# Performance work log

Measured on AMD Instinct MI355X. Metric: run time of the kernel, lower is better.

Reference implementation:

```python
import jax, jax.numpy as jnp
import numpy as np

H = 2880      # hidden_size
NH = 64       # num query heads
NKV = 8       # num kv heads
D = 64        # head_dim
G = NH // NKV # GQA group size
W = 128       # sliding window (keys per query, incl. self)
THETA = 150000.0
N = 1024      # tokens


def setup_inputs() -> dict:
    key = jax.random.key(0)
    k0, k1, k2, k3 = jax.random.split(key, 4)
    hidden_states = jax.random.normal(k0, (N, H), jnp.float32)
    Wqkv = jax.random.normal(k1, (H, (NH + 2 * NKV) * D), jnp.float32) * (H ** -0.5)
    Wo = jax.random.normal(k2, (NH * D, H), jnp.float32) * ((NH * D) ** -0.5)
    sinks = jax.random.normal(k3, (NH,), jnp.float32)
    positions = jnp.arange(N, dtype=jnp.int64)
    return {"hidden_states": hidden_states, "Wqkv": Wqkv, "Wo": Wo,
            "sinks": sinks, "positions": positions}


def _rope(x, pos):
    # NeoX-style rotary over full head_dim. x: [n, h, D], pos: [n]
    half = D // 2
    inv_freq = 1.0 / (THETA ** (jnp.arange(half, dtype=jnp.float32) / half))
    ang = pos[:, None].astype(jnp.float32) * inv_freq          # [n, half]
    cos = jnp.cos(ang)[:, None, :]
    sin = jnp.sin(ang)[:, None, :]
    x1, x2 = x[..., :half], x[..., half:]
    return jnp.concatenate([x1 * cos - x2 * sin, x2 * cos + x1 * sin], axis=-1)


def reference(hidden_states, Wqkv, Wo, sinks, positions):
    n = hidden_states.shape[0]
    qkv = hidden_states @ Wqkv
    q, k, v = jnp.split(qkv, [NH * D, NH * D + NKV * D], axis=-1)
    q = _rope(q.reshape(n, NH, D), positions)   # [n, NH, D]
    k = _rope(k.reshape(n, NKV, D), positions)  # [n, NKV, D]
    v = v.reshape(n, NKV, D)

    # Sliding-window key indices: query i attends keys j in [i-W+1, i]
    idx = positions[:, None] - (W - 1) + jnp.arange(W)[None, :]  # [n, W]
    valid = idx >= 0
    idx = jnp.clip(idx, 0, n - 1)
    k_win = k[idx]  # [n, W, NKV, D]
    v_win = v[idx]  # [n, W, NKV, D]

    qg = q.reshape(n, NKV, G, D)
    scores = jnp.einsum('nkgd,nwkd->nkgw', qg, k_win) * (D ** -0.5)
    scores = jnp.where(valid[:, None, None, :], scores, -jnp.inf)

    # Attention sinks: softmax over [scores, sink_logit]; sink gets no value.
    sink = sinks.reshape(NKV, G)                      # [NKV, G]
    m = jnp.maximum(scores.max(-1), sink[None])       # [n, NKV, G]
    p = jnp.exp(scores - m[..., None])                # [n, NKV, G, W]
    denom = p.sum(-1) + jnp.exp(sink[None] - m)       # [n, NKV, G]
    out = jnp.einsum('nkgw,nwkd->nkgd', p, v_win) / denom[..., None]
    return out.reshape(n, NH * D) @ Wo
```

## Files before the change

### kernel.cpp

```cpp
#include <hip/hip_runtime.h>
#include <hip/hip_bf16.h>

#define HDIM   2880
#define NH     64
#define NKV    8
#define DHEAD  64
#define GQ     (NH / NKV)
#define WIN    128
#define NTOK   1024
#define QKV_N  ((NH + 2 * NKV) * DHEAD)
#define QCOLS  (NH * DHEAD)
#define KOFF   QCOLS
#define VOFF   (QCOLS + NKV * DHEAD)
#define WO_PAD 2944

typedef __attribute__((ext_vector_type(8))) short short8;
typedef __attribute__((ext_vector_type(4))) float floatx4;

__device__ unsigned short g_Xb   [(size_t)NTOK  * HDIM];
__device__ float          g_qkv  [(size_t)NTOK  * QKV_N];
__device__ unsigned short g_attn [(size_t)NTOK  * QCOLS];
__device__ unsigned short g_WqkvT[(size_t)QKV_N * HDIM];
__device__ unsigned short g_WoT  [(size_t)WO_PAD * QCOLS];

__device__ __forceinline__ unsigned short f2b(float f) {
    __hip_bfloat16 h = __float2bfloat16(f);
    return *reinterpret_cast<unsigned short*>(&h);
}

__device__ __forceinline__ void gload_lds16(const unsigned short* g, unsigned short* l) {
    __builtin_amdgcn_global_load_lds(
        (const __attribute__((address_space(1))) unsigned int*)g,
        (__attribute__((address_space(3))) unsigned int*)l, 16, 0, 0);
}

__global__ __launch_bounds__(256) void transpose_cvt(
        const float* __restrict__ in, unsigned short* __restrict__ out,
        int K, int N) {
    int bk = blockIdx.x, bn = blockIdx.y;
    int t = threadIdx.x;
    __shared__ __align__(16) unsigned short T[64 * 72];
    #pragma unroll
    for (int i = 0; i < 4; ++i) {
        int c = i * 256 + t;
        int r = c >> 4, cc = (c & 15) * 4;
        float4 v = *(const float4*)(in + (size_t)(bk * 64 + r) * N + bn * 64 + cc);
        T[r * 72 + cc + 0] = f2b(v.x);
        T[r * 72 + cc + 1] = f2b(v.y);
        T[r * 72 + cc + 2] = f2b(v.z);
        T[r * 72 + cc + 3] = f2b(v.w);
    }
    __syncthreads();
    #pragma unroll
    for (int i = 0; i < 2; ++i) {
        int c = i * 256 + t;
        int rn = c >> 3, kc = (c & 7) * 8;
        int4 vv;
        unsigned short* tp = (unsigned short*)&vv;
        #pragma unroll
        for (int j = 0; j < 8; ++j) tp[j] = T[(kc + j) * 72 + rn];
        *(int4*)(out + (size_t)(bn * 64 + rn) * K + bk * 64 + kc) = vv;
    }
}

__global__ __launch_bounds__(256) void cvt_bf16(
        const float* __restrict__ in, unsigned short* __restrict__ out, int n4) {
    int id = blockIdx.x * 256 + threadIdx.x;
    if (id >= n4) return;
    float4 v = *(const float4*)(in + (size_t)id * 4);
    ushort4 o;
    o.x = f2b(v.x); o.y = f2b(v.y); o.z = f2b(v.z); o.w = f2b(v.w);
    *(ushort4*)(out + (size_t)id * 4) = o;
}

__global__ __launch_bounds__(256) void gemm64(
        const unsigned short* __restrict__ A, const unsigned short* __restrict__ Bt,
        float* __restrict__ C, int M, int N, int K) {
    int bm = blockIdx.x, bn = blockIdx.y;
    int t = threadIdx.x, lane = t & 63, wid = t >> 6;
    int quad = lane >> 4, ml = lane & 15;
    int wm = wid >> 1, wn = wid & 1;
    __shared__ __align__(16) unsigned short As[64 * 64];
    __shared__ __align__(16) unsigned short Bs[128 * 64];
    floatx4 acc[2][4];
    #pragma unroll
    for (int i = 0; i < 2; ++i)
        #pragma unroll
        for (int j = 0; j < 4; ++j) acc[i][j] = (floatx4){0.f, 0.f, 0.f, 0.f};

    int srow = lane >> 3;
    int scol = (lane & 7) * 8;
    const unsigned short* Ab = A  + (size_t)(bm * 64)  * K;
    const unsigned short* Bb = Bt + (size_t)(bn * 128) * K;

    for (int k0 = 0; k0 < K; k0 += 64) {
        #pragma unroll
        for (int j = 0; j < 2; ++j) {
            int grp = wid * 2 + j;
            int r = grp * 8 + srow;
            gload_lds16(Ab + (size_t)r * K + k0 + scol, &As[grp * 512]);
        }
        #pragma unroll
        for (int j = 0; j < 4; ++j) {
            int grp = wid * 4 + j;
            int r = grp * 8 + srow;
            gload_lds16(Bb + (size_t)r * K + k0 + scol, &Bs[grp * 512]);
        }
        __syncthreads();
        #pragma unroll
        for (int kk = 0; kk < 64; kk += 32) {
            short8 af[2], bf[4];
            #pragma unroll
            for (int mt = 0; mt < 2; ++mt)
                af[mt] = *(const short8*)&As[(wm * 32 + mt * 16 + ml) * 64 + kk + quad * 8];
            #pragma unroll
            for (int nt = 0; nt < 4; ++nt)
                bf[nt] = *(const short8*)&Bs[(wn * 64 + nt * 16 + ml) * 64 + kk + quad * 8];
            #pragma unroll
            for (int mt = 0; mt < 2; ++mt)
                #pragma unroll
                for (int nt = 0; nt < 4; ++nt)
                    acc[mt][nt] = __builtin_amdgcn_mfma_f32_16x16x32_bf16(af[mt], bf[nt], acc[mt][nt], 0, 0, 0);
        }
        __syncthreads();
    }
    #pragma unroll
    for (int mt = 0; mt < 2; ++mt)
        #pragma unroll
        for (int nt = 0; nt < 4; ++nt)
            #pragma unroll
            for (int r = 0; r < 4; ++r) {
                int row = bm * 64 + wm * 32 + mt * 16 + quad * 4 + r;
                int col = bn * 128 + wn * 64 + nt * 16 + ml;
                if (col < N) C[(size_t)row * N + col] = acc[mt][nt][r];
            }
}

__global__ __launch_bounds__(256) void rope_kernel(float* __restrict__ qkv) {
    int id = blockIdx.x * 256 + threadIdx.x;
    const int total = NTOK * (NH + NKV) * (DHEAD / 2);
    if (id >= total) return;
    int n = id / ((NH + NKV) * 32);
    int r = id - n * ((NH + NKV) * 32);
    int h = r >> 5, d = r & 31;
    int col = (h < NH) ? (h * DHEAD + d) : (KOFF + (h - NH) * DHEAD + d);
    size_t base = (size_t)n * QKV_N + col;
    float x1 = qkv[base];
    float x2 = qkv[base + 32];
    float inv = expf(-(float)d * 0.3724497053f);
    float ang = (float)n * inv;
    float s, c;
    sincosf(ang, &s, &c);
    qkv[base]      = x1 * c - x2 * s;
    qkv[base + 32] = x2 * c + x1 * s;
}

#define TQ     32
#define WROWS  160
#define KS_LD  72
#define VT_LD  168
#define PS_LD  168

__global__ __launch_bounds__(256) void attn_mfma(
        const float* __restrict__ qkv,
        const float* __restrict__ sinks,
        unsigned short* __restrict__ aout) {
    int t0 = blockIdx.x * TQ, kh = blockIdx.y;
    int t = threadIdx.x, lane = t & 63, wid = t >> 6;
    int quad = lane >> 4, ml = lane & 15;
    int wavebase = wid * 64;

    __shared__ __align__(16) unsigned short Ks[WROWS * KS_LD];
    __shared__ __align__(16) unsigned short Vt[DHEAD * VT_LD];
    __shared__ __align__(16) unsigned short Ps[4 * 16 * PS_LD];
    unsigned short* Psw = &Ps[wid * 16 * PS_LD];

    #pragma unroll
    for (int i = 0; i < 10; ++i) {
        int c = i * 256 + t;
        int w = c >> 4, dc = (c & 15) * 4;
        int r = t0 - 127 + w;
        r = min(max(r, 0), NTOK - 1);
        const float* kp = qkv + (size_t)r * QKV_N + KOFF + kh * DHEAD + dc;
        float4 kv = *(const float4*)kp;
        ushort4 kb;
        kb.x = f2b(kv.x); kb.y = f2b(kv.y); kb.z = f2b(kv.z); kb.w = f2b(kv.w);
        *(ushort4*)&Ks[w * KS_LD + dc] = kb;
        const float* vp = qkv + (size_t)r * QKV_N + VOFF + kh * DHEAD + dc;
        float4 vv = *(const float4*)vp;
        Vt[(dc + 0) * VT_LD + w] = f2b(vv.x);
        Vt[(dc + 1) * VT_LD + w] = f2b(vv.y);
        Vt[(dc + 2) * VT_LD + w] = f2b(vv.z);
        Vt[(dc + 3) * VT_LD + w] = f2b(vv.w);
    }
    __syncthreads();

    short8 qf[4][2];
    #pragma unroll
    for (int mt = 0; mt < 4; ++mt) {
        int m = wavebase + mt * 16 + ml;
        int tl = m & 31, g = m >> 5;
        const float* qp = qkv + (size_t)(t0 + tl) * QKV_N + (kh * GQ + g) * DHEAD;
        #pragma unroll
        for (int kk = 0; kk < 2; ++kk) {
            float4 a = *(const float4*)(qp + kk * 32 + quad * 8);
            float4 b = *(const float4*)(qp + kk * 32 + quad * 8 + 4);
            union { short8 s; unsigned short u[8]; } pk;
            pk.u[0] = f2b(a.x); pk.u[1] = f2b(a.y); pk.u[2] = f2b(a.z); pk.u[3] = f2b(a.w);
            pk.u[4] = f2b(b.x); pk.u[5] = f2b(b.y); pk.u[6] = f2b(b.z); pk.u[7] = f2b(b.w);
            qf[mt][kk] = pk.s;
        }
    }

    floatx4 S[4][10];
    #pragma unroll
    for (int mt = 0; mt < 4; ++mt)
        #pragma unroll
        for (int nt = 0; nt < 10; ++nt) S[mt][nt] = (floatx4){0.f, 0.f, 0.f, 0.f};
    #pragma unroll
    for (int kk = 0; kk < 2; ++kk) {
        #pragma unroll
        for (int nt = 0; nt < 10; ++nt) {
            short8 kb = *(const short8*)&Ks[(nt * 16 + ml) * KS_LD + kk * 32 + quad * 8];
            #pragma unroll
            for (int mt = 0; mt < 4; ++mt)
                S[mt][nt] = __builtin_amdgcn_mfma_f32_16x16x32_bf16(qf[mt][kk], kb, S[mt][nt], 0, 0, 0);
        }
    }

    int wmin0 = 127 - t0;
    #pragma unroll
    for (int mt = 0; mt < 4; ++mt) {
        #pragma unroll
        for (int r = 0; r < 4; ++r) {
            int tl = (wavebase + mt * 16 + quad * 4 + r) & 31;
            int wlo = tl > wmin0 ? tl : wmin0;
            int whi = tl + 127;
            #pragma unroll
            for (int nt = 0; nt < 10; ++nt) {
                int w = nt * 16 + ml;
                float s = S[mt][nt][r] * 0.125f;
                S[mt][nt][r] = (w >= wlo && w <= whi) ? s : -INFINITY;
            }
        }
    }

    #pragma unroll
    for (int mt = 0; mt < 4; ++mt) {
        int g = (wavebase + mt * 16) >> 5;
        float sk = sinks[kh * GQ + g];
        #pragma unroll
        for (int r = 0; r < 4; ++r) {
            float rm = -INFINITY;
            #pragma unroll
            for (int nt = 0; nt < 10; ++nt) rm = fmaxf(rm, S[mt][nt][r]);
            #pragma unroll
            for (int off = 1; off < 16; off <<= 1) rm = fmaxf(rm, __shfl_xor(rm, off));
            rm = fmaxf(rm, sk);
            float sum = 0.f;
            #pragma unroll
            for (int nt = 0; nt < 10; ++nt) {
                float p = __expf(S[mt][nt][r] - rm);
                S[mt][nt][r] = p;
                sum += p;
            }
            #pragma unroll
            for (int off = 1; off < 16; off <<= 1) sum += __shfl_xor(sum, off);
            float inv = 1.f / (sum + __expf(sk - rm));
            #pragma unroll
            for (int nt = 0; nt < 10; ++nt) S[mt][nt][r] *= inv;
        }
    }

    #pragma unroll
    for (int mt = 0; mt < 4; ++mt) {
        int m = wavebase + mt * 16;
        #pragma unroll
        for (int r = 0; r < 4; ++r) {
            int lr = quad * 4 + r;
            #pragma unroll
            for (int nt = 0; nt < 10; ++nt)
                Psw[lr * PS_LD + nt * 16 + ml] = f2b(S[mt][nt][r]);
        }
        floatx4 O[4];
        #pragma unroll
        for (int j = 0; j < 4; ++j) O[j] = (floatx4){0.f, 0.f, 0.f, 0.f};
        #pragma unroll
        for (int ks = 0; ks < 5; ++ks) {
            short8 pf = *(const short8*)&Psw[ml * PS_LD + ks * 32 + quad * 8];
            #pragma unroll
            for (int nt = 0; nt < 4; ++nt) {
                short8 vf = *(const short8*)&Vt[(nt * 16 + ml) * VT_LD + ks * 32 + quad * 8];
                O[nt] = __builtin_amdgcn_mfma_f32_16x16x32_bf16(pf, vf, O[nt], 0, 0, 0);
            }
        }
        #pragma unroll
        for (int r = 0; r < 4; ++r) {
            int mm = m + quad * 4 + r;
            int tl = mm & 31, g = mm >> 5;
            unsigned short* op = aout + (size_t)(t0 + tl) * QCOLS + (kh * GQ + g) * DHEAD;
            #pragma unroll
            for (int nt = 0; nt < 4; ++nt)
                op[nt * 16 + ml] = f2b(O[nt][r]);
        }
    }
}

extern "C" void kernel_launch(void* const* d_in, const int* in_sizes, int n_in,
                              void* d_out, int out_size, void* d_ws, size_t ws_size,
                              hipStream_t stream) {
    const float* X     = (const float*)d_in[0];
    const float* Wqkv  = (const float*)d_in[1];
    const float* Wo    = (const float*)d_in[2];
    const float* sinks = (const float*)d_in[3];
    float* out = (float*)d_out;

    unsigned short *Xb = nullptr, *attn = nullptr, *WqkvT = nullptr, *WoT = nullptr;
    float *qkv = nullptr;
    hipGetSymbolAddress((void**)&Xb,    HIP_SYMBOL(g_Xb));
    hipGetSymbolAddress((void**)&qkv,   HIP_SYMBOL(g_qkv));
    hipGetSymbolAddress((void**)&attn,  HIP_SYMBOL(g_attn));
    hipGetSymbolAddress((void**)&WqkvT, HIP_SYMBOL(g_WqkvT));
    hipGetSymbolAddress((void**)&WoT,   HIP_SYMBOL(g_WoT));

    cvt_bf16<<<(NTOK * HDIM / 4 + 255) / 256, 256, 0, stream>>>(X, Xb, NTOK * HDIM / 4);
    transpose_cvt<<<dim3(HDIM / 64, QKV_N / 64), 256, 0, stream>>>(Wqkv, WqkvT, HDIM, QKV_N);
    transpose_cvt<<<dim3(QCOLS / 64, HDIM / 64), 256, 0, stream>>>(Wo, WoT, QCOLS, HDIM);

    gemm64<<<dim3(NTOK / 64, QKV_N / 128), 256, 0, stream>>>(Xb, WqkvT, qkv, NTOK, QKV_N, HDIM);

    rope_kernel<<<(NTOK * (NH + NKV) * 32) / 256, 256, 0, stream>>>(qkv);

    attn_mfma<<<dim3(NTOK / TQ, NKV), 256, 0, stream>>>(qkv, sinks, attn);

    gemm64<<<dim3(NTOK / 64, WO_PAD / 128), 256, 0, stream>>>(attn, WoT, out, NTOK, HDIM, QCOLS);
}
```

Measured before the change: 348.5 us.

## Split-K GEMMs with fused reduce+RoPE, bf16 qkv, smaller attention tiles

Both GEMMs now use 128x128 tiles with split-K (3 and 4 slices) writing fp32 partial planes. A separate reduce kernel sums the partials, and for the QKV projection it also applies RoPE and stores qkv as bf16. Attention reads the bf16 qkv directly and uses 16-token tiles, giving twice as many blocks. The aim is more parallelism on a small-M problem and less fp32 qkv traffic, at the cost of extra partial-buffer writes and reads plus reduction launches.

New measurement: 333.0 us. 1.05x faster.

```diff
diff --git a/kernel.cpp b/kernel.cpp
--- a/kernel.cpp
+++ b/kernel.cpp
@@ -13,15 +13,19 @@
 #define KOFF   QCOLS
 #define VOFF   (QCOLS + NKV * DHEAD)
 #define WO_PAD 2944
+#define SK1    3
+#define SK2    4
 
 typedef __attribute__((ext_vector_type(8))) short short8;
 typedef __attribute__((ext_vector_type(4))) float floatx4;
 
 __device__ unsigned short g_Xb   [(size_t)NTOK  * HDIM];
-__device__ float          g_qkv  [(size_t)NTOK  * QKV_N];
+__device__ unsigned short g_qkvb [(size_t)NTOK  * QKV_N];
 __device__ unsigned short g_attn [(size_t)NTOK  * QCOLS];
 __device__ unsigned short g_WqkvT[(size_t)QKV_N * HDIM];
 __device__ unsigned short g_WoT  [(size_t)WO_PAD * QCOLS];
+__device__ float          g_part1[(size_t)SK1 * NTOK * QKV_N];
+__device__ float          g_part2[(size_t)SK2 * NTOK * WO_PAD];
 
 __device__ __forceinline__ unsigned short f2b(float f) {
     __hip_bfloat16 h = __float2bfloat16(f);
@@ -73,102 +77,151 @@
     *(ushort4*)(out + (size_t)id * 4) = o;
 }
 
-__global__ __launch_bounds__(256) void gemm64(
+__global__ __launch_bounds__(256) void gemm_sk(
         const unsigned short* __restrict__ A, const unsigned short* __restrict__ Bt,
-        float* __restrict__ C, int M, int N, int K) {
-    int bm = blockIdx.x, bn = blockIdx.y;
+        float* __restrict__ P, int K, int chunk, int ldc, size_t plane) {
+    int bm = blockIdx.x, bn = blockIdx.y, z = blockIdx.z;
     int t = threadIdx.x, lane = t & 63, wid = t >> 6;
     int quad = lane >> 4, ml = lane & 15;
     int wm = wid >> 1, wn = wid & 1;
-    __shared__ __align__(16) unsigned short As[64 * 64];
+    __shared__ __align__(16) unsigned short As[128 * 64];
     __shared__ __align__(16) unsigned short Bs[128 * 64];
-    floatx4 acc[2][4];
-    #pragma unroll
-    for (int i = 0; i < 2; ++i)
+    floatx4 acc[4][4];
+    #pragma unroll
+    for (int i = 0; i < 4; ++i)
         #pragma unroll
         for (int j = 0; j < 4; ++j) acc[i][j] = (floatx4){0.f, 0.f, 0.f, 0.f};
 
     int srow = lane >> 3;
     int scol = (lane & 7) * 8;
-    const unsigned short* Ab = A  + (size_t)(bm * 64)  * K;
-    const unsigned short* Bb = Bt + (size_t)(bn * 128) * K;
-
-    for (int k0 = 0; k0 < K; k0 += 64) {
-        #pragma unroll
-        for (int j = 0; j < 2; ++j) {
-            int grp = wid * 2 + j;
-            int r = grp * 8 + srow;
-            gload_lds16(Ab + (size_t)r * K + k0 + scol, &As[grp * 512]);
-        }
+    int base = z * chunk;
+    const unsigned short* Ab = A  + (size_t)(bm * 128) * K + base;
+    const unsigned short* Bb = Bt + (size_t)(bn * 128) * K + base;
+
+    for (int k0 = 0; k0 < chunk; k0 += 64) {
         #pragma unroll
         for (int j = 0; j < 4; ++j) {
             int grp = wid * 4 + j;
             int r = grp * 8 + srow;
+            gload_lds16(Ab + (size_t)r * K + k0 + scol, &As[grp * 512]);
             gload_lds16(Bb + (size_t)r * K + k0 + scol, &Bs[grp * 512]);
         }
         __syncthreads();
         #pragma unroll
         for (int kk = 0; kk < 64; kk += 32) {
-            short8 af[2], bf[4];
-            #pragma unroll
-            for (int mt = 0; mt < 2; ++mt)
-                af[mt] = *(const short8*)&As[(wm * 32 + mt * 16 + ml) * 64 + kk + quad * 8];
+            short8 af[4], bf[4];
+            #pragma unroll
+            for (int mt = 0; mt < 4; ++mt)
+                af[mt] = *(const short8*)&As[(wm * 64 + mt * 16 + ml) * 64 + kk + quad * 8];
             #pragma unroll
             for (int nt = 0; nt < 4; ++nt)
                 bf[nt] = *(const short8*)&Bs[(wn * 64 + nt * 16 + ml) * 64 + kk + quad * 8];
             #pragma unroll
-            for (int mt = 0; mt < 2; ++mt)
+            for (int mt = 0; mt < 4; ++mt)
                 #pragma unroll
                 for (int nt = 0; nt < 4; ++nt)
                     acc[mt][nt] = __builtin_amdgcn_mfma_f32_16x16x32_bf16(af[mt], bf[nt], acc[mt][nt], 0, 0, 0);
         }
         __syncthreads();
     }
-    #pragma unroll
-    for (int mt = 0; mt < 2; ++mt)
+    float* Cp = P + z * plane;
+    #pragma unroll
+    for (int mt = 0; mt < 4; ++mt)
         #pragma unroll
         for (int nt = 0; nt < 4; ++nt)
             #pragma unroll
             for (int r = 0; r < 4; ++r) {
-                int row = bm * 64 + wm * 32 + mt * 16 + quad * 4 + r;
+                int row = bm * 128 + wm * 64 + mt * 16 + quad * 4 + r;
                 int col = bn * 128 + wn * 64 + nt * 16 + ml;
-                if (col < N) C[(size_t)row * N + col] = acc[mt][nt][r];
+                Cp[(size_t)row * ldc + col] = acc[mt][nt][r];
             }
 }
 
-__global__ __launch_bounds__(256) void rope_kernel(float* __restrict__ qkv) {
+#define QK_UNITS (NTOK * 72 * 8)
+#define V_UNITS  (NTOK * 128)
+__global__ __launch_bounds__(256) void reduce_rope(
+        const float* __restrict__ P, unsigned short* __restrict__ qkvb) {
     int id = blockIdx.x * 256 + threadIdx.x;
-    const int total = NTOK * (NH + NKV) * (DHEAD / 2);
-    if (id >= total) return;
-    int n = id / ((NH + NKV) * 32);
-    int r = id - n * ((NH + NKV) * 32);
-    int h = r >> 5, d = r & 31;
-    int col = (h < NH) ? (h * DHEAD + d) : (KOFF + (h - NH) * DHEAD + d);
-    size_t base = (size_t)n * QKV_N + col;
-    float x1 = qkv[base];
-    float x2 = qkv[base + 32];
-    float inv = expf(-(float)d * 0.3724497053f);
-    float ang = (float)n * inv;
-    float s, c;
-    sincosf(ang, &s, &c);
-    qkv[base]      = x1 * c - x2 * s;
-    qkv[base + 32] = x2 * c + x1 * s;
-}
-
-#define TQ     32
+    const size_t plane = (size_t)NTOK * QKV_N;
+    if (id < QK_UNITS) {
+        int n = id / 576;
+        int rem = id - n * 576;
+        int hh = rem >> 3, q8 = rem & 7;
+        int c0 = (hh < NH) ? hh * 64 : KOFF + (hh - NH) * 64;
+        size_t i1 = (size_t)n * QKV_N + c0 + q8 * 4;
+        float4 a0 = *(const float4*)(P + i1);
+        float4 a1 = *(const float4*)(P + plane + i1);
+        float4 a2 = *(const float4*)(P + 2 * plane + i1);
+        float4 b0 = *(const float4*)(P + i1 + 32);
+        float4 b1 = *(const float4*)(P + plane + i1 + 32);
+        float4 b2 = *(const float4*)(P + 2 * plane + i1 + 32);
+        float x1[4] = {a0.x + a1.x + a2.x, a0.y + a1.y + a2.y,
+                       a0.z + a1.z + a2.z, a0.w + a1.w + a2.w};
+        float x2[4] = {b0.x + b1.x + b2.x, b0.y + b1.y + b2.y,
+                       b0.z + b1.z + b2.z, b0.w + b1.w + b2.w};
+        union { ushort4 v; unsigned short u[4]; } o1, o2;
+        #pragma unroll
+        for (int j = 0; j < 4; ++j) {
+            int d = q8 * 4 + j;
+            float inv = expf(-(float)d * 0.3724497053f);
+            float ang = (float)n * inv;
+            float s, c;
+            sincosf(ang, &s, &c);
+            o1.u[j] = f2b(x1[j] * c - x2[j] * s);
+            o2.u[j] = f2b(x2[j] * c + x1[j] * s);
+        }
+        *(ushort4*)(qkvb + i1) = o1.v;
+        *(ushort4*)(qkvb + i1 + 32) = o2.v;
+    } else if (id < QK_UNITS + V_UNITS) {
+        int vid = id - QK_UNITS;
+        int n = vid >> 7, s8 = vid & 127;
+        size_t i1 = (size_t)n * QKV_N + VOFF + s8 * 4;
+        float4 a0 = *(const float4*)(P + i1);
+        float4 a1 = *(const float4*)(P + plane + i1);
+        float4 a2 = *(const float4*)(P + 2 * plane + i1);
+        union { ushort4 v; unsigned short u[4]; } o;
+        o.u[0] = f2b(a0.x + a1.x + a2.x);
+        o.u[1] = f2b(a0.y + a1.y + a2.y);
+        o.u[2] = f2b(a0.z + a1.z + a2.z);
+        o.u[3] = f2b(a0.w + a1.w + a2.w);
+        *(ushort4*)(qkvb + i1) = o.v;
+    }
+}
+
+__global__ __launch_bounds__(256) void reduce_out(
+        const float* __restrict__ P, float* __restrict__ out) {
+    int id = blockIdx.x * 256 + threadIdx.x;
+    if (id >= NTOK * (HDIM / 4)) return;
+    int n = id / (HDIM / 4);
+    int c = (id - n * (HDIM / 4)) * 4;
+    const size_t plane = (size_t)NTOK * WO_PAD;
+    size_t i = (size_t)n * WO_PAD + c;
+    float4 a0 = *(const float4*)(P + i);
+    float4 a1 = *(const float4*)(P + plane + i);
+    float4 a2 = *(const float4*)(P + 2 * plane + i);
+    float4 a3 = *(const float4*)(P + 3 * plane + i);
+    float4 s;
+    s.x = a0.x + a1.x + a2.x + a3.x;
+    s.y = a0.y + a1.y + a2.y + a3.y;
+    s.z = a0.z + a1.z + a2.z + a3.z;
+    s.w = a0.w + a1.w + a2.w + a3.w;
+    *(float4*)(out + (size_t)n * HDIM + c) = s;
+}
+
+#define TQ     16
 #define WROWS  160
 #define KS_LD  72
 #define VT_LD  168
 #define PS_LD  168
 
 __global__ __launch_bounds__(256) void attn_mfma(
-        const float* __restrict__ qkv,
+        const unsigned short* __restrict__ qkvb,
         const float* __restrict__ sinks,
         unsigned short* __restrict__ aout) {
     int t0 = blockIdx.x * TQ, kh = blockIdx.y;
     int t = threadIdx.x, lane = t & 63, wid = t >> 6;
     int quad = lane >> 4, ml = lane & 15;
-    int wavebase = wid * 64;
+    int wavebase = wid * 32;
 
     __shared__ __align__(16) unsigned short Ks[WROWS * KS_LD];
     __shared__ __align__(16) unsigned short Vt[DHEAD * VT_LD];
@@ -176,45 +229,34 @@
     unsigned short* Psw = &Ps[wid * 16 * PS_LD];
 
     #pragma unroll
-    for (int i = 0; i < 10; ++i) {
+    for (int i = 0; i < 5; ++i) {
         int c = i * 256 + t;
-        int w = c >> 4, dc = (c & 15) * 4;
+        int w = c >> 3, d8 = (c & 7) * 8;
         int r = t0 - 127 + w;
         r = min(max(r, 0), NTOK - 1);
-        const float* kp = qkv + (size_t)r * QKV_N + KOFF + kh * DHEAD + dc;
-        float4 kv = *(const float4*)kp;
-        ushort4 kb;
-        kb.x = f2b(kv.x); kb.y = f2b(kv.y); kb.z = f2b(kv.z); kb.w = f2b(kv.w);
-        *(ushort4*)&Ks[w * KS_LD + dc] = kb;
-        const float* vp = qkv + (size_t)r * QKV_N + VOFF + kh * DHEAD + dc;
-        float4 vv = *(const float4*)vp;
-        Vt[(dc + 0) * VT_LD + w] = f2b(vv.x);
-        Vt[(dc + 1) * VT_LD + w] = f2b(vv.y);
-        Vt[(dc + 2) * VT_LD + w] = f2b(vv.z);
-        Vt[(dc + 3) * VT_LD + w] = f2b(vv.w);
+        *(int4*)&Ks[w * KS_LD + d8] =
+            *(const int4*)(qkvb + (size_t)r * QKV_N + KOFF + kh * DHEAD + d8);
+        int4 vv = *(const int4*)(qkvb + (size_t)r * QKV_N + VOFF + kh * DHEAD + d8);
+        const unsigned short* vp = (const unsigned short*)&vv;
+        #pragma unroll
+        for (int j = 0; j < 8; ++j) Vt[(d8 + j) * VT_LD + w] = vp[j];
     }
     __syncthreads();
 
-    short8 qf[4][2];
-    #pragma unroll
-    for (int mt = 0; mt < 4; ++mt) {
+    short8 qf[2][2];
+    #pragma unroll
+    for (int mt = 0; mt < 2; ++mt) {
         int m = wavebase + mt * 16 + ml;
-        int tl = m & 31, g = m >> 5;
-        const float* qp = qkv + (size_t)(t0 + tl) * QKV_N + (kh * GQ + g) * DHEAD;
-        #pragma unroll
-        for (int kk = 0; kk < 2; ++kk) {
-            float4 a = *(const float4*)(qp + kk * 32 + quad * 8);
-            float4 b = *(const float4*)(qp + kk * 32 + quad * 8 + 4);
-            union { short8 s; unsigned short u[8]; } pk;
-            pk.u[0] = f2b(a.x); pk.u[1] = f2b(a.y); pk.u[2] = f2b(a.z); pk.u[3] = f2b(a.w);
-            pk.u[4] = f2b(b.x); pk.u[5] = f2b(b.y); pk.u[6] = f2b(b.z); pk.u[7] = f2b(b.w);
-            qf[mt][kk] = pk.s;
-        }
-    }
-
-    floatx4 S[4][10];
-    #pragma unroll
-    for (int mt = 0; mt < 4; ++mt)
+        int tl = m & 15, g = m >> 4;
+        const unsigned short* qp = qkvb + (size_t)(t0 + tl) * QKV_N + (kh * GQ + g) * DHEAD;
+        #pragma unroll
+        for (int kk = 0; kk < 2; ++kk)
+            qf[mt][kk] = *(const short8*)(qp + kk * 32 + quad * 8);
+    }
+
+    floatx4 S[2][10];
+    #pragma unroll
+    for (int mt = 0; mt < 2; ++mt)
         #pragma unroll
         for (int nt = 0; nt < 10; ++nt) S[mt][nt] = (floatx4){0.f, 0.f, 0.f, 0.f};
     #pragma unroll
@@ -223,17 +265,17 @@
         for (int nt = 0; nt < 10; ++nt) {
             short8 kb = *(const short8*)&Ks[(nt * 16 + ml) * KS_LD + kk * 32 + quad * 8];
             #pragma unroll
-            for (int mt = 0; mt < 4; ++mt)
+            for (int mt = 0; mt < 2; ++mt)
                 S[mt][nt] = __builtin_amdgcn_mfma_f32_16x16x32_bf16(qf[mt][kk], kb, S[mt][nt], 0, 0, 0);
         }
     }
 
     int wmin0 = 127 - t0;
     #pragma unroll
-    for (int mt = 0; mt < 4; ++mt) {
+    for (int mt = 0; mt < 2; ++mt) {
         #pragma unroll
         for (int r = 0; r < 4; ++r) {
-            int tl = (wavebase + mt * 16 + quad * 4 + r) & 31;
+            int tl = (wavebase + mt * 16 + quad * 4 + r) & 15;
             int wlo = tl > wmin0 ? tl : wmin0;
             int whi = tl + 127;
             #pragma unroll
@@ -246,8 +288,8 @@
     }
 
     #pragma unroll
-    for (int mt = 0; mt < 4; ++mt) {
-        int g = (wavebase + mt * 16) >> 5;
+    for (int mt = 0; mt < 2; ++mt) {
+        int g = (wavebase + mt * 16) >> 4;
         float sk = sinks[kh * GQ + g];
         #pragma unroll
         for (int r = 0; r < 4; ++r) {
@@ -273,8 +315,7 @@
     }
 
     #pragma unroll
-    for (int mt = 0; mt < 4; ++mt) {
-        int m = wavebase + mt * 16;
+    for (int mt = 0; mt < 2; ++mt) {
         #pragma unroll
         for (int r = 0; r < 4; ++r) {
             int lr = quad * 4 + r;
@@ -296,8 +337,8 @@
         }
         #pragma unroll
         for (int r = 0; r < 4; ++r) {
-            int mm = m + quad * 4 + r;
-            int tl = mm & 31, g = mm >> 5;
+            int mm = wavebase + mt * 16 + quad * 4 + r;
+            int tl = mm & 15, g = mm >> 4;
             unsigned short* op = aout + (size_t)(t0 + tl) * QCOLS + (kh * GQ + g) * DHEAD;
             #pragma unroll
             for (int nt = 0; nt < 4; ++nt)
@@ -315,23 +356,29 @@
     const float* sinks = (const float*)d_in[3];
     float* out = (float*)d_out;
 
-    unsigned short *Xb = nullptr, *attn = nullptr, *WqkvT = nullptr, *WoT = nullptr;
-    float *qkv = nullptr;
+    unsigned short *Xb, *qkvb, *attn, *WqkvT, *WoT;
+    float *part1, *part2;
     hipGetSymbolAddress((void**)&Xb,    HIP_SYMBOL(g_Xb));
-    hipGetSymbolAddress((void**)&qkv,   HIP_SYMBOL(g_qkv));
+    hipGetSymbolAddress((void**)&qkvb,  HIP_SYMBOL(g_qkvb));
     hipGetSymbolAddress((void**)&attn,  HIP_SYMBOL(g_attn));
     hipGetSymbolAddress((void**)&WqkvT, HIP_SYMBOL(g_WqkvT));
     hipGetSymbolAddress((void**)&WoT,   HIP_SYMBOL(g_WoT));
+    hipGetSymbolAddress((void**)&part1, HIP_SYMBOL(g_part1));
+    hipGetSymbolAddress((void**)&part2, HIP_SYMBOL(g_part2));
 
     cvt_bf16<<<(NTOK * HDIM / 4 + 255) / 256, 256, 0, stream>>>(X, Xb, NTOK * HDIM / 4);
     transpose_cvt<<<dim3(HDIM / 64, QKV_N / 64), 256, 0, stream>>>(Wqkv, WqkvT, HDIM, QKV_N);
     transpose_cvt<<<dim3(QCOLS / 64, HDIM / 64), 256, 0, stream>>>(Wo, WoT, QCOLS, HDIM);
 
-    gemm64<<<dim3(NTOK / 64, QKV_N / 128), 256, 0, stream>>>(Xb, WqkvT, qkv, NTOK, QKV_N, HDIM);
-
-    rope_kernel<<<(NTOK * (NH + NKV) * 32) / 256, 256, 0, stream>>>(qkv);
-
-    attn_mfma<<<dim3(NTOK / TQ, NKV), 256, 0, stream>>>(qkv, sinks, attn);
-
-    gemm64<<<dim3(NTOK / 64, WO_PAD / 128), 256, 0, stream>>>(attn, WoT, out, NTOK, HDIM, QCOLS);
-}
+    gemm_sk<<<dim3(NTOK / 128, QKV_N / 128, SK1), 256, 0, stream>>>(
+        Xb, WqkvT, part1, HDIM, HDIM / SK1, QKV_N, (size_t)NTOK * QKV_N);
+
+    reduce_rope<<<(QK_UNITS + V_UNITS) / 256, 256, 0, stream>>>(part1, qkvb);
+
+    attn_mfma<<<dim3(NTOK / TQ, NKV), 256, 0, stream>>>(qkvb, sinks, attn);
+
+    gemm_sk<<<dim3(NTOK / 128, WO_PAD / 128, SK2), 256, 0, stream>>>(
+        attn, WoT, part2, QCOLS, QCOLS / SK2, WO_PAD, (size_t)NTOK * WO_PAD);
+
+    reduce_out<<<(NTOK * (HDIM / 4) + 255) / 256, 256, 0, stream>>>(part2, out);
+}
```
